# Performance work log

Hardware: AMD Instinct MI355X
Metric: run time of the kernel (lower is better)

Reference implementation:

```python
import jax, jax.numpy as jnp
import numpy as np

T_VAL = 256.0   # t_val = 2**8
EPS = 1e-05
N_BANDS = 128
B, C, T = 16, 1, 2048


def setup_inputs() -> dict:
    key = jax.random.key(0)
    k_x, = jax.random.split(key, 1)
    x = jax.random.uniform(k_x, (B, C, N_BANDS, T), dtype=jnp.float32)
    # learned params stored in log-space, as in the torch module
    alpha = jnp.full((N_BANDS,), np.log(0.8), dtype=jnp.float32)
    delta = jnp.full((N_BANDS,), np.log(10.0), dtype=jnp.float32)
    r = jnp.full((N_BANDS,), np.log(0.25), dtype=jnp.float32)
    return {"x": x, "alpha": alpha, "delta": delta, "r": r}


def reference(x, alpha, delta, r):
    # smoothing coefficient from t_val
    s = (jnp.sqrt(1.0 + 4.0 * T_VAL ** 2) - 1.0) / (2.0 * T_VAL ** 2)
    a = jnp.exp(alpha)[:, None]   # [n_bands, 1]
    d = jnp.exp(delta)[:, None]
    rr = jnp.exp(r)[:, None]

    n = x.shape[-1]
    # v[i, j] = (1-s)^(j - i) for j >= i, else 0   (upper-triangular [n, n])
    p = (1.0 - s) ** jnp.arange(n + 1, dtype=x.dtype)          # [n+1]
    v = jnp.triu(jnp.tile(p, n).reshape(n + 1, n)[:-1])        # [n, n]

    # IIR/EMA smoother expressed as dense triangular matmul (as in source)
    # smoother[..., t] = s * sum_k x[..., k] v[k, t] + (1-s) * x[..., 0] v[0, t]
    smoother = s * (x @ v) + (1.0 - s) * x[..., 0, None] @ v[None, 0]

    # smooth = (eps + smoother)^(-alpha), computed stably in log space
    smooth = jnp.exp(-a * (jnp.log(EPS) + jnp.log1p(smoother / EPS)))
    pcen = (x * smooth + d) ** rr - d ** rr                    # [B, C, n_bands, T]
    return jnp.transpose(pcen, (0, 1, 3, 2))                   # [B, C, T, n_bands]
```

## Files before the change

kernel.cpp:

```cpp
#include <hip/hip_runtime.h>
#include <math.h>


#define T_LEN   2048
#define NBANDS  128
#define PLANE   2120

__global__ __launch_bounds__(512) void pcen_kernel(
    const float* __restrict__ x,
    const float* __restrict__ alpha,
    const float* __restrict__ delta,
    const float* __restrict__ r,
    float* __restrict__ out)
{
    __shared__ float tile[8 * PLANE];

    const int tid  = threadIdx.x;
    const int w    = tid >> 6;
    const int lane = tid & 63;
    const int bid  = blockIdx.x;
    const int b    = bid >> 4;
    const int bg   = bid & 15;
    const int band = bg * 8 + w;

    const float s = (sqrtf(262145.0f) - 1.0f) / 131072.0f;
    const float g = 1.0f - s;
    float g32 = g * g;
    g32 *= g32;
    g32 *= g32;
    g32 *= g32;
    g32 *= g32;

    const float a    = __expf(alpha[band]);
    const float dd   = __expf(delta[band]);
    const float rr   = __expf(r[band]);
    const float dpow = __expf(rr * delta[band]);
    const float LOG_EPS = -11.512925465f;
    const float INV_EPS = 1.0e5f;

    const size_t row = ((size_t)b * NBANDS + band) * T_LEN;
    const float* xp  = x + row + (size_t)lane * 32;

    float xs[32];
    #pragma unroll
    for (int j = 0; j < 8; ++j) {
        const float4 v4 = *reinterpret_cast<const float4*>(xp + j * 4);
        xs[j*4+0] = v4.x; xs[j*4+1] = v4.y; xs[j*4+2] = v4.z; xs[j*4+3] = v4.w;
    }

    float m = (lane == 0) ? xs[0] : 0.0f;
    #pragma unroll
    for (int k = 0; k < 32; ++k) m = fmaf(g, m, s * xs[k]);

    float v = m;
    float f = g32;
    #pragma unroll
    for (int off = 1; off < 64; off <<= 1) {
        float u = __shfl_up(v, off, 64);
        if (lane >= off) v = fmaf(f, u, v);
        f = f * f;
    }
    float carry = __shfl_up(v, 1, 64);
    if (lane == 0) carry = xs[0];

    float* tw = tile + w * PLANE + lane * 33;
    m = carry;
    #pragma unroll
    for (int k = 0; k < 32; ++k) {
        m = fmaf(g, m, s * xs[k]);
        float lg     = LOG_EPS + __logf(fmaf(m, INV_EPS, 1.0f));
        float smooth = __expf(-a * lg);
        float base   = fmaf(xs[k], smooth, dd);
        float o      = __expf(rr * __logf(base)) - dpow;
        tw[k] = o;
    }
    __syncthreads();

    const int wp  = tid & 7;
    const int tof = tid >> 3;
    float* op = out + (size_t)b * T_LEN * NBANDS + bg * 8;
    #pragma unroll 4
    for (int c = 0; c < 32; ++c) {
        int t = c * 64 + tof;
        int l = t >> 5;
        int k = t & 31;
        op[(size_t)t * NBANDS + wp] = tile[wp * PLANE + l * 33 + k];
    }
}

extern "C" void kernel_launch(void* const* d_in, const int* in_sizes, int n_in,
                              void* d_out, int out_size, void* d_ws, size_t ws_size,
                              hipStream_t stream) {
    const float* x     = (const float*)d_in[0];
    const float* alpha = (const float*)d_in[1];
    const float* delta = (const float*)d_in[2];
    const float* r     = (const float*)d_in[3];
    float* out = (float*)d_out;

    hipLaunchKernelGGL(pcen_kernel, dim3(16 * 16), dim3(512), 0, stream,
                       x, alpha, delta, r, out);
}
```

Baseline: 81.54 us.

## Split each band's scan across two waves with cross-wave carry via LDS

```diff
diff --git a/kernel.cpp b/kernel.cpp
--- a/kernel.cpp
+++ b/kernel.cpp
@@ -4,32 +4,34 @@
 
 #define T_LEN   2048
 #define NBANDS  128
-#define PLANE   2120
+#define PL      2184
 
-__global__ __launch_bounds__(512) void pcen_kernel(
+__global__ __launch_bounds__(1024) void pcen_kernel(
     const float* __restrict__ x,
     const float* __restrict__ alpha,
     const float* __restrict__ delta,
     const float* __restrict__ r,
     float* __restrict__ out)
 {
-    __shared__ float tile[8 * PLANE];
+    __shared__ float tile[8 * PL];
+    __shared__ float carr[8];
 
     const int tid  = threadIdx.x;
     const int w    = tid >> 6;
     const int lane = tid & 63;
+    const int wb   = w & 7;
+    const int h    = w >> 3;
     const int bid  = blockIdx.x;
     const int b    = bid >> 4;
     const int bg   = bid & 15;
-    const int band = bg * 8 + w;
+    const int band = bg * 8 + wb;
 
     const float s = (sqrtf(262145.0f) - 1.0f) / 131072.0f;
     const float g = 1.0f - s;
-    float g32 = g * g;
-    g32 *= g32;
-    g32 *= g32;
-    g32 *= g32;
-    g32 *= g32;
+    float g16 = g * g;
+    g16 *= g16;
+    g16 *= g16;
+    g16 *= g16;
 
     const float a    = __expf(alpha[band]);
     const float dd   = __expf(delta[band]);
@@ -39,21 +41,21 @@
     const float INV_EPS = 1.0e5f;
 
     const size_t row = ((size_t)b * NBANDS + band) * T_LEN;
-    const float* xp  = x + row + (size_t)lane * 32;
+    const float* xp  = x + row + (size_t)h * 1024 + (size_t)lane * 16;
 
-    float xs[32];
+    float xs[16];
     #pragma unroll
-    for (int j = 0; j < 8; ++j) {
+    for (int j = 0; j < 4; ++j) {
         const float4 v4 = *reinterpret_cast<const float4*>(xp + j * 4);
         xs[j*4+0] = v4.x; xs[j*4+1] = v4.y; xs[j*4+2] = v4.z; xs[j*4+3] = v4.w;
     }
 
-    float m = (lane == 0) ? xs[0] : 0.0f;
+    float m = (h == 0 && lane == 0) ? xs[0] : 0.0f;
     #pragma unroll
-    for (int k = 0; k < 32; ++k) m = fmaf(g, m, s * xs[k]);
+    for (int k = 0; k < 16; ++k) m = fmaf(g, m, s * xs[k]);
 
     float v = m;
-    float f = g32;
+    float f = g16;
     #pragma unroll
     for (int off = 1; off < 64; off <<= 1) {
         float u = __shfl_up(v, off, 64);
@@ -61,12 +63,21 @@
         f = f * f;
     }
     float carry = __shfl_up(v, 1, 64);
-    if (lane == 0) carry = xs[0];
+    if (lane == 0) carry = (h == 0) ? xs[0] : 0.0f;
 
-    float* tw = tile + w * PLANE + lane * 33;
+    if (h == 0 && lane == 63) carr[wb] = v;
+    __syncthreads();
+    if (h == 1) {
+        const float m1023 = carr[wb];
+        const float lng16 = __logf(g16);
+        const float scale = __expf((float)lane * lng16);
+        carry = fmaf(scale, m1023, carry);
+    }
+
+    float* tw = tile + wb * PL + (h * 64 + lane) * 17;
     m = carry;
     #pragma unroll
-    for (int k = 0; k < 32; ++k) {
+    for (int k = 0; k < 16; ++k) {
         m = fmaf(g, m, s * xs[k]);
         float lg     = LOG_EPS + __logf(fmaf(m, INV_EPS, 1.0f));
         float smooth = __expf(-a * lg);
@@ -80,11 +91,11 @@
     const int tof = tid >> 3;
     float* op = out + (size_t)b * T_LEN * NBANDS + bg * 8;
     #pragma unroll 4
-    for (int c = 0; c < 32; ++c) {
-        int t = c * 64 + tof;
-        int l = t >> 5;
-        int k = t & 31;
-        op[(size_t)t * NBANDS + wp] = tile[wp * PLANE + l * 33 + k];
+    for (int c = 0; c < 16; ++c) {
+        int t = c * 128 + tof;
+        int l = t >> 4;
+        int k = t & 15;
+        op[(size_t)t * NBANDS + wp] = tile[wp * PL + l * 17 + k];
     }
 }
 
@@ -97,6 +108,6 @@
     const float* r     = (const float*)d_in[3];
     float* out = (float*)d_out;
 
-    hipLaunchKernelGGL(pcen_kernel, dim3(16 * 16), dim3(512), 0, stream,
+    hipLaunchKernelGGL(pcen_kernel, dim3(16 * 16), dim3(1024), 0, stream,
                        x, alpha, delta, r, out);
 }
```

After: 82.06 us. No clear change (+0.6%).
